# Kernel optimization log

Measured on AMD Instinct MI355X. Metric: run time of the kernel, lower is better.

The kernel has to match this reference:

```python
import jax, jax.numpy as jnp
import numpy as np

WIDTH, DEPTH = 2048, 8
TIME_MOD = 30 * DEPTH + 2  # 242


def setup_inputs() -> dict:
    key = jax.random.key(0)
    ks = jax.random.split(key, 7)
    s = float(np.sqrt(1.0 / WIDTH))
    so = float(np.sqrt(1.0 / (WIDTH + DEPTH + 1)))
    return {
        "x": jax.random.normal(ks[0], (WIDTH,), dtype=jnp.float32),
        "weights": jax.random.uniform(ks[1], (WIDTH, WIDTH, DEPTH), minval=-s, maxval=s, dtype=jnp.float32),
        "output_weights": jax.random.uniform(ks[2], (WIDTH, DEPTH + 1), minval=-so, maxval=so, dtype=jnp.float32),
        "state": jax.random.uniform(ks[3], (WIDTH, DEPTH + 1), dtype=jnp.float32),  # relu outputs >= 0
        "stored_activations": jax.random.uniform(ks[4], (WIDTH, DEPTH + 1, TIME_MOD), dtype=jnp.float32),
        "stored_gradiets": jax.random.normal(ks[5], (WIDTH, DEPTH), dtype=jnp.float32),
        "output_gradient": jax.random.normal(ks[6], (WIDTH, DEPTH + 1, TIME_MOD), dtype=jnp.float32),
        "time": 7,
    }


def reference(x, weights, output_weights, state, stored_activations, stored_gradiets, output_gradient, time):
    width, dp1 = state.shape
    depth = dp1 - 1
    mod = 30 * depth + 2
    dt = state.dtype

    # recurrent state update: state[w,d] = relu(sum_i weights[i,w,d] * state_prev[i,d])
    hidden = jax.nn.relu(jnp.einsum("iwd,id->wd", weights, state[:, :depth]))
    state = jnp.concatenate([x[:, None], hidden], axis=1)  # (W, depth+1)
    output = jnp.sum(output_weights * state)

    # scatter into circular buffers at slot `time` (static int)
    sa = stored_activations.at[:, :, time].set(state)
    og = output_gradient.at[:, :, time].set(output_weights)

    # stored gradients: loop over a reads only OLD stored_gradiets[:, a+1] -> vectorizable
    a = np.arange(depth - 1)  # a = 0 .. depth-2 (static indices)
    t_idx = (time - 2 * depth + 2 * (a + 1)) % mod  # (depth-1,)
    relu_m = (sa[:, a + 2, (t_idx + 1) % mod] > 0).astype(dt)  # (W, depth-1)
    contrib = jnp.einsum("ija,ja->ia", weights[:, :, 1:depth], stored_gradiets[:, 1:depth])
    sg_head = relu_m * contrib + og[:, a + 1, t_idx]  # (W, depth-1)
    sg_last = og[:, depth, time]  # a == depth-1 branch (time_index == time)
    sg = jnp.concatenate([sg_head, sg_last[:, None]], axis=1)  # (W, depth)

    output_weights_gradient = state

    # weight eligibility traces (uses UPDATED sa and UPDATED sg)
    aa = np.arange(depth)
    tia = (time - 2 * depth + 2 * (aa + 1)) % mod  # (depth,)
    relu_g = (sa[:, aa + 1, tia] > 0).astype(dt)  # (W, depth)
    act_prev = sa[:, aa, (tia - 1) % mod]  # (W, depth)
    gradients = act_prev[:, None, :] * (sg * relu_g)[None, :, :]  # (W, W, depth)

    return output, state, sa, sg, og, gradients, output_weights_gradient
```

## Files before the change

kernel.cpp:

```cpp
#include <hip/hip_runtime.h>

#define MOD 242

static constexpr long long OFF_STATE = 1;
static constexpr long long OFF_SA    = 18433;
static constexpr long long OFF_SG    = 4478977;
static constexpr long long OFF_OG    = 4495361;
static constexpr long long OFF_GRAD  = 8955905;
static constexpr long long OFF_OWG   = 42510337;

#define WS_HID 0
#define WS_CON 16384
#define WS_COL 32768
#define WS_ROW 49152

__global__ __launch_bounds__(256) void k_matvec(
    const float* __restrict__ weights, const float* __restrict__ state,
    const float* __restrict__ sgrad, float* __restrict__ ws)
{
  const int b  = blockIdx.x;
  const int i0 = (b & 31) * 64;
  const int w0 = (b >> 5) * 128;
  const int tid = threadIdx.x;
  const int wv  = tid >> 6;
  const int l   = tid & 63;
  const int d4  = l & 1;
  const int w   = w0 + wv * 32 + (l >> 1);

  __shared__ __align__(16) float state_lds[64 * 8];
  __shared__ __align__(16) float contrib_lds[4][64][8];

  for (int idx = tid; idx < 64 * 8; idx += 256)
    state_lds[idx] = state[(size_t)(i0 + (idx >> 3)) * 9 + (idx & 7)];
  for (int idx = tid; idx < 4 * 64 * 8; idx += 256)
    (&contrib_lds[0][0][0])[idx] = 0.0f;
  __syncthreads();

  const float4 sg4 = *(const float4*)&sgrad[(size_t)w * 8 + d4 * 4];
  float4 h4 = make_float4(0.f, 0.f, 0.f, 0.f);
  const float* wp = weights + ((size_t)i0 * 2048 + w) * 8 + d4 * 4;

  #pragma unroll 4
  for (int ii = 0; ii < 64; ++ii) {
    const float4 w4 = *(const float4*)wp;
    wp += 16384;
    const float4 s4 = *(const float4*)&state_lds[ii * 8 + d4 * 4];
    h4.x = fmaf(w4.x, s4.x, h4.x);
    h4.y = fmaf(w4.y, s4.y, h4.y);
    h4.z = fmaf(w4.z, s4.z, h4.z);
    h4.w = fmaf(w4.w, s4.w, h4.w);

    float vx = w4.x * sg4.x, vy = w4.y * sg4.y, vz = w4.z * sg4.z, vw = w4.w * sg4.w;
    #pragma unroll
    for (int m = 2; m <= 32; m <<= 1) {
      vx += __shfl_xor(vx, m);
      vy += __shfl_xor(vy, m);
      vz += __shfl_xor(vz, m);
      vw += __shfl_xor(vw, m);
    }
    if (l < 2) {
      float4* p = (float4*)&contrib_lds[wv][ii][l * 4];
      float4 o = *p;
      o.x += vx; o.y += vy; o.z += vz; o.w += vw;
      *p = o;
    }
  }

  atomicAdd(&ws[WS_HID + w * 8 + d4 * 4 + 0], h4.x);
  atomicAdd(&ws[WS_HID + w * 8 + d4 * 4 + 1], h4.y);
  atomicAdd(&ws[WS_HID + w * 8 + d4 * 4 + 2], h4.z);
  atomicAdd(&ws[WS_HID + w * 8 + d4 * 4 + 3], h4.w);

  __syncthreads();
  for (int idx = tid; idx < 64 * 8; idx += 256) {
    const int ii = idx >> 3, d = idx & 7;
    const float s = contrib_lds[0][ii][d] + contrib_lds[1][ii][d]
                  + contrib_lds[2][ii][d] + contrib_lds[3][ii][d];
    atomicAdd(&ws[WS_CON + (i0 + ii) * 8 + d], s);
  }
}

__global__ __launch_bounds__(256) void k_copy2(
    const float* __restrict__ a, float* __restrict__ da,
    const float* __restrict__ b, float* __restrict__ db, int n)
{
  const int stride = gridDim.x * blockDim.x;
  for (int i = blockIdx.x * blockDim.x + threadIdx.x; i < n; i += stride) {
    da[i] = a[i];
    db[i] = b[i];
  }
}

__global__ __launch_bounds__(256) void k_finalize(
    const float* __restrict__ x, const float* __restrict__ ow,
    const float* __restrict__ sa_in, const float* __restrict__ og_in,
    const int* __restrict__ timep, float* __restrict__ ws, float* __restrict__ out)
{
  const int r = blockIdx.x * 256 + threadIdx.x;
  const int t = *timep;

  float s[9];
  s[0] = x[r];
  const float4 hA = *(const float4*)&ws[WS_HID + r * 8];
  const float4 hB = *(const float4*)&ws[WS_HID + r * 8 + 4];
  s[1] = fmaxf(hA.x, 0.f); s[2] = fmaxf(hA.y, 0.f);
  s[3] = fmaxf(hA.z, 0.f); s[4] = fmaxf(hA.w, 0.f);
  s[5] = fmaxf(hB.x, 0.f); s[6] = fmaxf(hB.y, 0.f);
  s[7] = fmaxf(hB.z, 0.f); s[8] = fmaxf(hB.w, 0.f);

  float owr[9];
  #pragma unroll
  for (int c = 0; c < 9; ++c) owr[c] = ow[(size_t)r * 9 + c];

  float p = 0.f;
  #pragma unroll
  for (int c = 0; c < 9; ++c) {
    out[OFF_STATE + (size_t)r * 9 + c] = s[c];
    out[OFF_OWG   + (size_t)r * 9 + c] = s[c];
    out[OFF_SA + ((size_t)r * 9 + c) * MOD + t] = s[c];
    out[OFF_OG + ((size_t)r * 9 + c) * MOD + t] = owr[c];
    p = fmaf(owr[c], s[c], p);
  }
  #pragma unroll
  for (int m = 1; m < 64; m <<= 1) p += __shfl_xor(p, m);
  if ((threadIdx.x & 63) == 0) atomicAdd(out, p);

  float con[8];
  const float4 cA = *(const float4*)&ws[WS_CON + r * 8];
  const float4 cB = *(const float4*)&ws[WS_CON + r * 8 + 4];
  con[0] = cA.x; con[1] = cA.y; con[2] = cA.z; con[3] = cA.w;
  con[4] = cB.x; con[5] = cB.y; con[6] = cB.z; con[7] = cB.w;

  float sg[8];
  #pragma unroll
  for (int a = 0; a < 7; ++a) {
    const int ti = (t + 2 * a - 14 + MOD) % MOD;
    const int tm = (ti + 1) % MOD;
    const float av  = (tm == t) ? s[a + 2] : sa_in[((size_t)r * 9 + a + 2) * MOD + tm];
    const float ogv = (ti == t) ? owr[a + 1] : og_in[((size_t)r * 9 + a + 1) * MOD + ti];
    sg[a] = (av > 0.f ? con[a + 1] : 0.f) + ogv;
  }
  sg[7] = owr[8];
  #pragma unroll
  for (int a = 0; a < 8; ++a) out[OFF_SG + (size_t)r * 8 + a] = sg[a];

  #pragma unroll
  for (int aa = 0; aa < 8; ++aa) {
    const int ti = (t + 2 * aa - 14 + MOD) % MOD;
    const int tp = (ti - 1 + MOD) % MOD;
    const float rv = (ti == t) ? s[aa + 1] : sa_in[((size_t)r * 9 + aa + 1) * MOD + ti];
    const float ap = (tp == t) ? s[aa]     : sa_in[((size_t)r * 9 + aa) * MOD + tp];
    ws[WS_COL + r * 8 + aa] = (rv > 0.f) ? sg[aa] : 0.f;
    ws[WS_ROW + r * 8 + aa] = ap;
  }
}

__global__ __launch_bounds__(256) void k_grad(
    const float* __restrict__ ws, float* __restrict__ out)
{
  const int i = blockIdx.x;
  const int tid = threadIdx.x;
  const float rf = ws[WS_ROW + i * 8 + (tid & 7)];
  float* o = out + OFF_GRAD + (size_t)i * 16384;
  const float* cf = ws + WS_COL;
  #pragma unroll 4
  for (int k = 0; k < 64; ++k) {
    const int e = k * 256 + tid;
    o[e] = rf * cf[e];
  }
}

extern "C" void kernel_launch(void* const* d_in, const int* in_sizes, int n_in,
                              void* d_out, int out_size, void* d_ws, size_t ws_size,
                              hipStream_t stream)
{
  (void)in_sizes; (void)n_in; (void)out_size; (void)ws_size;
  const float* x     = (const float*)d_in[0];
  const float* wts   = (const float*)d_in[1];
  const float* ow    = (const float*)d_in[2];
  const float* st    = (const float*)d_in[3];
  const float* sa_in = (const float*)d_in[4];
  const float* sgrad = (const float*)d_in[5];
  const float* og_in = (const float*)d_in[6];
  const int*   timep = (const int*)d_in[7];
  float* out = (float*)d_out;
  float* ws  = (float*)d_ws;

  hipMemsetAsync(ws, 0, 32768 * sizeof(float), stream);
  hipMemsetAsync(out, 0, sizeof(float), stream);

  k_matvec<<<512, 256, 0, stream>>>(wts, st, sgrad, ws);
  k_copy2<<<2048, 256, 0, stream>>>(sa_in, out + OFF_SA, og_in, out + OFF_OG, 4460544);
  k_finalize<<<8, 256, 0, stream>>>(x, ow, sa_in, og_in, timep, ws, out);
  k_grad<<<2048, 256, 0, stream>>>(ws, out);
}
```

Measured before the change: 363.6 us.

## Replace atomics and memsets with partial-sum buffers and DPP wave reductions

The matvec kernel now writes per-block partial sums for the hidden state and the contribution vector into separate workspace slices instead of atomically adding into one zeroed buffer. This removes both memsets and the global atomics. Each wave now handles 64 consecutive columns for one half of the depth, so the cross-lane reduction uses DPP row operations instead of shuffles. The finalize kernel sums the partials (32 per element for hidden, 16 for contrib) and writes per-block scalar outputs, which the grad kernel then sums into the scalar result. The copy kernel uses one element per thread with no loop. The trade-off is a larger workspace and extra reduction reads in the small finalize kernel.

```diff
diff --git a/kernel.cpp b/kernel.cpp
--- a/kernel.cpp
+++ b/kernel.cpp
@@ -9,104 +9,130 @@
 static constexpr long long OFF_GRAD  = 8955905;
 static constexpr long long OFF_OWG   = 42510337;
 
-#define WS_HID 0
-#define WS_CON 16384
-#define WS_COL 32768
-#define WS_ROW 49152
+#define WS_HID  0
+#define WS_CON  524288
+#define WS_COL  786432
+#define WS_ROW  802816
+#define WS_OUTP 819200
+
+template <int CTRL, int RM>
+__device__ __forceinline__ float dppadd(float x) {
+  int t = __builtin_amdgcn_update_dpp(0, __float_as_int(x), CTRL, RM, 0xF, true);
+  return x + __int_as_float(t);
+}
+__device__ __forceinline__ float wave_sum_dpp(float x) {
+  x = dppadd<0x111, 0xF>(x);
+  x = dppadd<0x112, 0xF>(x);
+  x = dppadd<0x114, 0xF>(x);
+  x = dppadd<0x118, 0xF>(x);
+  x = dppadd<0x142, 0xA>(x);
+  x = dppadd<0x143, 0xC>(x);
+  return x;
+}
 
 __global__ __launch_bounds__(256) void k_matvec(
     const float* __restrict__ weights, const float* __restrict__ state,
     const float* __restrict__ sgrad, float* __restrict__ ws)
 {
-  const int b  = blockIdx.x;
-  const int i0 = (b & 31) * 64;
-  const int w0 = (b >> 5) * 128;
-  const int tid = threadIdx.x;
-  const int wv  = tid >> 6;
-  const int l   = tid & 63;
-  const int d4  = l & 1;
-  const int w   = w0 + wv * 32 + (l >> 1);
+  const int b    = blockIdx.x;
+  const int iblk = b & 31;
+  const int wblk = b >> 5;
+  const int i0   = iblk * 64;
+  const int w0   = wblk * 128;
+  const int tid  = threadIdx.x;
+  const int wv   = tid >> 6;
+  const int l    = tid & 63;
+  const int wgrp = wv >> 1;
+  const int dh   = wv & 1;
+  const int w    = w0 + wgrp * 64 + l;
 
   __shared__ __align__(16) float state_lds[64 * 8];
-  __shared__ __align__(16) float contrib_lds[4][64][8];
+  __shared__ __align__(16) float cl[4][64][4];
 
   for (int idx = tid; idx < 64 * 8; idx += 256)
     state_lds[idx] = state[(size_t)(i0 + (idx >> 3)) * 9 + (idx & 7)];
-  for (int idx = tid; idx < 4 * 64 * 8; idx += 256)
-    (&contrib_lds[0][0][0])[idx] = 0.0f;
   __syncthreads();
 
-  const float4 sg4 = *(const float4*)&sgrad[(size_t)w * 8 + d4 * 4];
+  const float4 sg4 = *(const float4*)&sgrad[(size_t)w * 8 + dh * 4];
   float4 h4 = make_float4(0.f, 0.f, 0.f, 0.f);
-  const float* wp = weights + ((size_t)i0 * 2048 + w) * 8 + d4 * 4;
+  const float* wp = weights + ((size_t)i0 * 2048 + w) * 8 + dh * 4;
 
   #pragma unroll 4
   for (int ii = 0; ii < 64; ++ii) {
     const float4 w4 = *(const float4*)wp;
     wp += 16384;
-    const float4 s4 = *(const float4*)&state_lds[ii * 8 + d4 * 4];
+    const float4 s4 = *(const float4*)&state_lds[ii * 8 + dh * 4];
+
     h4.x = fmaf(w4.x, s4.x, h4.x);
     h4.y = fmaf(w4.y, s4.y, h4.y);
     h4.z = fmaf(w4.z, s4.z, h4.z);
     h4.w = fmaf(w4.w, s4.w, h4.w);
 
-    float vx = w4.x * sg4.x, vy = w4.y * sg4.y, vz = w4.z * sg4.z, vw = w4.w * sg4.w;
-    #pragma unroll
-    for (int m = 2; m <= 32; m <<= 1) {
-      vx += __shfl_xor(vx, m);
-      vy += __shfl_xor(vy, m);
-      vz += __shfl_xor(vz, m);
-      vw += __shfl_xor(vw, m);
-    }
-    if (l < 2) {
-      float4* p = (float4*)&contrib_lds[wv][ii][l * 4];
-      float4 o = *p;
-      o.x += vx; o.y += vy; o.z += vz; o.w += vw;
-      *p = o;
-    }
-  }
-
-  atomicAdd(&ws[WS_HID + w * 8 + d4 * 4 + 0], h4.x);
-  atomicAdd(&ws[WS_HID + w * 8 + d4 * 4 + 1], h4.y);
-  atomicAdd(&ws[WS_HID + w * 8 + d4 * 4 + 2], h4.z);
-  atomicAdd(&ws[WS_HID + w * 8 + d4 * 4 + 3], h4.w);
+    float vx = wave_sum_dpp(w4.x * sg4.x);
+    float vy = wave_sum_dpp(w4.y * sg4.y);
+    float vz = wave_sum_dpp(w4.z * sg4.z);
+    float vw = wave_sum_dpp(w4.w * sg4.w);
+    if (l == 63)
+      *(float4*)&cl[wv][ii][0] = make_float4(vx, vy, vz, vw);
+  }
+
+  *(float4*)&ws[WS_HID + ((size_t)iblk * 2048 + w) * 8 + dh * 4] = h4;
 
   __syncthreads();
-  for (int idx = tid; idx < 64 * 8; idx += 256) {
-    const int ii = idx >> 3, d = idx & 7;
-    const float s = contrib_lds[0][ii][d] + contrib_lds[1][ii][d]
-                  + contrib_lds[2][ii][d] + contrib_lds[3][ii][d];
-    atomicAdd(&ws[WS_CON + (i0 + ii) * 8 + d], s);
+  {
+    const int ii = tid >> 2, q = tid & 3;
+    const float c0 = cl[0][ii][q] + cl[2][ii][q];
+    const float c1 = cl[1][ii][q] + cl[3][ii][q];
+    const size_t base = WS_CON + ((size_t)wblk * 2048 + i0 + ii) * 8;
+    ws[base + q]     = c0;
+    ws[base + 4 + q] = c1;
   }
 }
 
 __global__ __launch_bounds__(256) void k_copy2(
     const float* __restrict__ a, float* __restrict__ da,
-    const float* __restrict__ b, float* __restrict__ db, int n)
-{
-  const int stride = gridDim.x * blockDim.x;
-  for (int i = blockIdx.x * blockDim.x + threadIdx.x; i < n; i += stride) {
-    da[i] = a[i];
-    db[i] = b[i];
-  }
-}
-
-__global__ __launch_bounds__(256) void k_finalize(
+    const float* __restrict__ b, float* __restrict__ db)
+{
+  const int i = blockIdx.x * 256 + threadIdx.x;
+  da[i] = a[i];
+  db[i] = b[i];
+}
+
+__global__ __launch_bounds__(64) void k_finalize(
     const float* __restrict__ x, const float* __restrict__ ow,
     const float* __restrict__ sa_in, const float* __restrict__ og_in,
     const int* __restrict__ timep, float* __restrict__ ws, float* __restrict__ out)
 {
-  const int r = blockIdx.x * 256 + threadIdx.x;
+  const int r = blockIdx.x * 64 + threadIdx.x;
   const int t = *timep;
+
+  float hid[8] = {0,0,0,0,0,0,0,0};
+  {
+    const float4* hp = (const float4*)&ws[WS_HID + (size_t)r * 8];
+    #pragma unroll
+    for (int ib = 0; ib < 32; ++ib) {
+      const float4 pa = hp[(size_t)ib * 4096];
+      const float4 pb = hp[(size_t)ib * 4096 + 1];
+      hid[0] += pa.x; hid[1] += pa.y; hid[2] += pa.z; hid[3] += pa.w;
+      hid[4] += pb.x; hid[5] += pb.y; hid[6] += pb.z; hid[7] += pb.w;
+    }
+  }
+  float con[8] = {0,0,0,0,0,0,0,0};
+  {
+    const float4* cp = (const float4*)&ws[WS_CON + (size_t)r * 8];
+    #pragma unroll
+    for (int wb = 0; wb < 16; ++wb) {
+      const float4 pa = cp[(size_t)wb * 4096];
+      const float4 pb = cp[(size_t)wb * 4096 + 1];
+      con[0] += pa.x; con[1] += pa.y; con[2] += pa.z; con[3] += pa.w;
+      con[4] += pb.x; con[5] += pb.y; con[6] += pb.z; con[7] += pb.w;
+    }
+  }
 
   float s[9];
   s[0] = x[r];
-  const float4 hA = *(const float4*)&ws[WS_HID + r * 8];
-  const float4 hB = *(const float4*)&ws[WS_HID + r * 8 + 4];
-  s[1] = fmaxf(hA.x, 0.f); s[2] = fmaxf(hA.y, 0.f);
-  s[3] = fmaxf(hA.z, 0.f); s[4] = fmaxf(hA.w, 0.f);
-  s[5] = fmaxf(hB.x, 0.f); s[6] = fmaxf(hB.y, 0.f);
-  s[7] = fmaxf(hB.z, 0.f); s[8] = fmaxf(hB.w, 0.f);
+  #pragma unroll
+  for (int d = 0; d < 8; ++d) s[d + 1] = fmaxf(hid[d], 0.f);
 
   float owr[9];
   #pragma unroll
@@ -123,13 +149,7 @@
   }
   #pragma unroll
   for (int m = 1; m < 64; m <<= 1) p += __shfl_xor(p, m);
-  if ((threadIdx.x & 63) == 0) atomicAdd(out, p);
-
-  float con[8];
-  const float4 cA = *(const float4*)&ws[WS_CON + r * 8];
-  const float4 cB = *(const float4*)&ws[WS_CON + r * 8 + 4];
-  con[0] = cA.x; con[1] = cA.y; con[2] = cA.z; con[3] = cA.w;
-  con[4] = cB.x; con[5] = cB.y; con[6] = cB.z; con[7] = cB.w;
+  if (threadIdx.x == 0) ws[WS_OUTP + blockIdx.x] = p;
 
   float sg[8];
   #pragma unroll
@@ -160,6 +180,12 @@
 {
   const int i = blockIdx.x;
   const int tid = threadIdx.x;
+  if (i == 0 && tid == 0) {
+    float s = 0.f;
+    #pragma unroll
+    for (int k = 0; k < 32; ++k) s += ws[WS_OUTP + k];
+    out[0] = s;
+  }
   const float rf = ws[WS_ROW + i * 8 + (tid & 7)];
   float* o = out + OFF_GRAD + (size_t)i * 16384;
   const float* cf = ws + WS_COL;
@@ -186,11 +212,8 @@
   float* out = (float*)d_out;
   float* ws  = (float*)d_ws;
 
-  hipMemsetAsync(ws, 0, 32768 * sizeof(float), stream);
-  hipMemsetAsync(out, 0, sizeof(float), stream);
-
   k_matvec<<<512, 256, 0, stream>>>(wts, st, sgrad, ws);
-  k_copy2<<<2048, 256, 0, stream>>>(sa_in, out + OFF_SA, og_in, out + OFF_OG, 4460544);
-  k_finalize<<<8, 256, 0, stream>>>(x, ow, sa_in, og_in, timep, ws, out);
+  k_copy2<<<17424, 256, 0, stream>>>(sa_in, out + OFF_SA, og_in, out + OFF_OG);
+  k_finalize<<<32, 64, 0, stream>>>(x, ow, sa_in, og_in, timep, ws, out);
   k_grad<<<2048, 256, 0, stream>>>(ws, out);
 }
```

Measured after the change: 343.9 us. -5.4%, faster.
